# Kernel tuning notes

Measured on AMD Instinct MI355X. Metric: run time of the kernel, lower is better.

Reference implementation:

```python
import jax, jax.numpy as jnp
from jax import lax
import numpy as np

TOP_K = 2
CAPACITY_FACTOR = 1.0


def setup_inputs() -> dict:
    key = jax.random.key(0)
    kx, kg, k1, k2 = jax.random.split(key, 4)
    B, S, D, F, E = 8, 4096, 512, 1024, 16
    x = jax.random.normal(kx, (B, S, D), dtype=jnp.float32)
    w_gate = jax.random.normal(kg, (D, E), dtype=jnp.float32) * 0.02
    w1 = jax.random.normal(k1, (E, D, 2 * F), dtype=jnp.float32) * 0.02
    w2 = jax.random.normal(k2, (E, F, D), dtype=jnp.float32) * 0.02
    return {"x": x, "w_gate": w_gate, "w1": w1, "w2": w2}


def reference(x, w_gate, w1, w2):
    # Inference mode: no gating noise, dropout is identity.
    B, S, D = x.shape
    E = w_gate.shape[1]
    T = B * S
    capacity = max(1, int(CAPACITY_FACTOR * T / E))  # static

    flat = x.reshape(T, D)
    gate_logits = flat @ w_gate                      # [T, E]
    gate_scores = jax.nn.softmax(gate_logits, axis=-1)
    topk_vals, topk_idx = lax.top_k(gate_scores, TOP_K)  # [T, k]

    phi_mean = gate_scores.mean(axis=0)
    aux_loss = E * jnp.sum(phi_mean * phi_mean)

    # Per-expert combine weight for every token: [E, T]
    onehot = topk_idx[None, :, :] == jnp.arange(E)[:, None, None]  # [E, T, k]
    w_et = jnp.sum(jnp.where(onehot, topk_vals[None], 0.0), axis=-1)  # [E, T]

    # Capacity truncation: keep the `capacity` highest-weight tokens per expert
    sel_w, sel_idx = lax.top_k(w_et, capacity)  # [E, C]; unrouted picks have weight 0

    xs = flat[sel_idx]                                  # [E, C, D] gather
    h = jnp.einsum('ecd,edf->ecf', xs, w1)              # [E, C, 2F]
    h1, h2 = jnp.split(h, 2, axis=-1)
    act = h1 * jax.nn.silu(h2)                          # SwiGLU
    out_e = jnp.einsum('ecf,efd->ecd', act, w2) * sel_w[..., None]  # [E, C, D]

    combined = jnp.zeros((T, D), dtype=flat.dtype).at[sel_idx.reshape(-1)].add(
        out_e.reshape(-1, D))
    return combined.reshape(B, S, D), aux_loss
```

## Files before the change

### kernel.cpp

```cpp
#include <hip/hip_runtime.h>
#include <hip/hip_bf16.h>
#include <math.h>

#define T_TOK 32768
#define D_DIM 512
#define E_EXP 16
#define F_DIM 1024
#define C_CAP 2048

typedef __attribute__((ext_vector_type(8))) __bf16 bf16x8;
typedef __attribute__((ext_vector_type(4))) float f32x4;

__device__ __forceinline__ unsigned short f2bf(float f) {
  unsigned u = __float_as_uint(f);
  u += 0x7FFFu + ((u >> 16) & 1u);
  return (unsigned short)(u >> 16);
}

__device__ __forceinline__ void gld16(const void* gptr, void* ldsptr) {
  __builtin_amdgcn_global_load_lds(
      (__attribute__((address_space(1))) void*)(void*)gptr,
      (__attribute__((address_space(3))) void*)ldsptr, 16, 0, 0);
}

__global__ void transpose_conv_kernel(const float* __restrict__ in,
                                      unsigned short* __restrict__ out,
                                      int R, int Cc) {
  __shared__ float tile[32][33];
  int e = blockIdx.z;
  int r0 = blockIdx.y * 32, c0 = blockIdx.x * 32;
  const float* pin = in + (size_t)e * R * Cc;
  unsigned short* pout = out + (size_t)e * R * Cc;
  int tx = threadIdx.x, ty = threadIdx.y;
  #pragma unroll
  for (int i = 0; i < 32; i += 8)
    tile[ty + i][tx] = pin[(size_t)(r0 + ty + i) * Cc + c0 + tx];
  __syncthreads();
  #pragma unroll
  for (int i = 0; i < 32; i += 8)
    pout[(size_t)(c0 + ty + i) * R + r0 + tx] = f2bf(tile[tx][ty + i]);
}

__global__ __launch_bounds__(256) void gate_kernel(
    const float* __restrict__ x, const float* __restrict__ wg,
    float* __restrict__ w_et, float* __restrict__ phi_sum,
    unsigned short* __restrict__ xb) {
  __shared__ float wgl[D_DIM * E_EXP];
  __shared__ float phil[E_EXP];
  int tid = threadIdx.x;
  for (int i = tid; i < D_DIM * E_EXP; i += 256) wgl[i] = wg[i];
  if (tid < E_EXP) phil[tid] = 0.f;
  __syncthreads();

  int g = tid >> 4;
  int e = tid & 15;
  int t = blockIdx.x * 16 + g;

  float acc = 0.f;
  const float* xr = x + (size_t)t * D_DIM;
  #pragma unroll 4
  for (int d = 0; d < D_DIM; d += 4) {
    float4 xv = *(const float4*)(xr + d);
    acc = fmaf(xv.x, wgl[(d + 0) * 16 + e], acc);
    acc = fmaf(xv.y, wgl[(d + 1) * 16 + e], acc);
    acc = fmaf(xv.z, wgl[(d + 2) * 16 + e], acc);
    acc = fmaf(xv.w, wgl[(d + 3) * 16 + e], acc);
  }

  unsigned short* xrow = xb + (size_t)t * D_DIM;
  #pragma unroll
  for (int j = 0; j < 8; ++j) {
    int idx = j * 16 + e;
    float4 v = *(const float4*)(xr + idx * 4);
    ushort4 o;
    o.x = f2bf(v.x); o.y = f2bf(v.y); o.z = f2bf(v.z); o.w = f2bf(v.w);
    ((ushort4*)xrow)[idx] = o;
  }

  float m = acc;
  for (int off = 8; off; off >>= 1) m = fmaxf(m, __shfl_xor(m, off));
  float p = expf(acc - m);
  float s = p;
  for (int off = 8; off; off >>= 1) s += __shfl_xor(s, off);
  float score = p / s;
  atomicAdd(&phil[e], score);

  float v1 = score; int i1 = e;
  for (int off = 8; off; off >>= 1) {
    float ov = __shfl_xor(v1, off); int oi = __shfl_xor(i1, off);
    if (ov > v1 || (ov == v1 && oi < i1)) { v1 = ov; i1 = oi; }
  }
  float sc2 = (e == i1) ? -1.f : score;
  float v2 = sc2; int i2 = e;
  for (int off = 8; off; off >>= 1) {
    float ov = __shfl_xor(v2, off); int oi = __shfl_xor(i2, off);
    if (ov > v2 || (ov == v2 && oi < i2)) { v2 = ov; i2 = oi; }
  }
  if (e == 0) {
    w_et[(size_t)i1 * T_TOK + t] = v1;
    w_et[(size_t)i2 * T_TOK + t] = v2;
  }
  __syncthreads();
  if (tid < E_EXP) atomicAdd(&phi_sum[tid], phil[tid]);
}

__global__ void aux_kernel(const float* __restrict__ phi_sum, float* __restrict__ out_aux) {
  if (threadIdx.x == 0) {
    float s = 0.f;
    for (int e = 0; e < E_EXP; ++e) {
      float pm = phi_sum[e] / (float)T_TOK;
      s += pm * pm;
    }
    *out_aux = (float)E_EXP * s;
  }
}

__global__ __launch_bounds__(1024) void select_kernel(
    const float* __restrict__ w_et, int* __restrict__ sel_idx, float* __restrict__ sel_w) {
  int e = blockIdx.x, tid = threadIdx.x;
  const float* w = w_et + (size_t)e * T_TOK;
  __shared__ unsigned hist[256];
  __shared__ unsigned scan_buf[1024];
  __shared__ unsigned sh_prefix, sh_k, sh_ngt, sh_cnt;

  unsigned prefix = 0, k = C_CAP, n_gt = 0;
  for (int pass = 0; pass < 4; ++pass) {
    int shift = 24 - pass * 8;
    if (tid < 256) hist[tid] = 0;
    if (tid == 0) sh_cnt = 0;
    __syncthreads();
    for (int i = tid; i < T_TOK; i += 1024) {
      unsigned b = __float_as_uint(w[i]);
      bool match = (pass == 0) || ((b >> (shift + 8)) == (prefix >> (shift + 8)));
      if (match) atomicAdd(&hist[(b >> shift) & 0xFFu], 1u);
    }
    __syncthreads();
    if (tid == 0) {
      unsigned cum = 0; int b = 255;
      for (; b > 0; --b) {
        unsigned c = hist[b];
        if (cum + c >= k) break;
        cum += c;
      }
      sh_prefix = prefix | ((unsigned)b << shift);
      sh_k = k - cum;
      sh_ngt = n_gt + cum;
    }
    __syncthreads();
    prefix = sh_prefix; k = sh_k; n_gt = sh_ngt;
    __syncthreads();
  }

  unsigned thr = prefix;
  unsigned eq_take = k;
  int base = tid * 32;

  unsigned myeq = 0;
  for (int i = base; i < base + 32; ++i) {
    float v = w[i];
    unsigned b = __float_as_uint(v);
    if (b > thr) {
      unsigned pos = atomicAdd(&sh_cnt, 1u);
      sel_idx[(size_t)e * C_CAP + pos] = i;
      sel_w[(size_t)e * C_CAP + pos] = v;
    } else if (b == thr) {
      myeq++;
    }
  }
  scan_buf[tid] = myeq;
  __syncthreads();
  for (int off = 1; off < 1024; off <<= 1) {
    unsigned add = (tid >= off) ? scan_buf[tid - off] : 0u;
    __syncthreads();
    scan_buf[tid] += add;
    __syncthreads();
  }
  unsigned excl = scan_buf[tid] - myeq;

  if (thr != 0u) {
    unsigned r = excl;
    for (int i = base; i < base + 32 && r < eq_take; ++i) {
      unsigned b = __float_as_uint(w[i]);
      if (b == thr) {
        sel_idx[(size_t)e * C_CAP + n_gt + r] = i;
        sel_w[(size_t)e * C_CAP + n_gt + r] = w[i];
        r++;
      }
    }
  }
  unsigned m_e = (thr != 0u) ? (unsigned)C_CAP : n_gt;
  for (unsigned i = m_e + tid; i < C_CAP; i += 1024) {
    sel_idx[(size_t)e * C_CAP + i] = 0;
    sel_w[(size_t)e * C_CAP + i] = 0.f;
  }
}

__global__ __launch_bounds__(256) void gemm1_kernel(
    const unsigned short* __restrict__ xb,
    const unsigned short* __restrict__ w1t,
    const int* __restrict__ sel_idx,
    unsigned short* __restrict__ act) {
  __shared__ __align__(16) unsigned short As[128 * 64];
  __shared__ __align__(16) unsigned short Bs[128 * 64];
  int bid = (blockIdx.x & 7) * 512 + (blockIdx.x >> 3);
  int nt = bid & 15, mt = (bid >> 4) & 15, e = bid >> 8;
  int tid = threadIdx.x, lane = tid & 63, wid = tid >> 6;

  const unsigned short* ag[4];
  const unsigned short* bg[4];
  unsigned lofs[4];
  #pragma unroll
  for (int s = 0; s < 4; ++s) {
    int c = s * 256 + tid;
    int row = c >> 3, kc = c & 7;
    int kcs = kc ^ (row & 7);
    int tok = sel_idx[e * C_CAP + mt * 128 + row];
    ag[s] = xb + (size_t)tok * D_DIM + kcs * 8;
    int hcol = (row < 64) ? (nt * 64 + row) : (F_DIM + nt * 64 + (row - 64));
    bg[s] = w1t + ((size_t)e * 2 * F_DIM + hcol) * D_DIM + kcs * 8;
    lofs[s] = (unsigned)(s * 256 + wid * 64) * 16;
  }

  f32x4 zero = {0.f, 0.f, 0.f, 0.f};
  f32x4 acc[2][8];
  #pragma unroll
  for (int m = 0; m < 2; ++m)
    #pragma unroll
    for (int n = 0; n < 8; ++n) acc[m][n] = zero;

  int cl = lane & 15, rg = lane >> 4;
  int sw = cl & 7;

  for (int kt = 0; kt < D_DIM / 64; ++kt) {
    #pragma unroll
    for (int s = 0; s < 4; ++s) {
      gld16(ag[s] + kt * 64, (char*)As + lofs[s]);
      gld16(bg[s] + kt * 64, (char*)Bs + lofs[s]);
    }
    __syncthreads();
    #pragma unroll
    for (int kk = 0; kk < 64; kk += 32) {
      int cofs = (((kk >> 3) + rg) ^ sw) << 3;
      bf16x8 a[2], b[8];
      #pragma unroll
      for (int m = 0; m < 2; ++m)
        a[m] = *(const bf16x8*)&As[(wid * 32 + m * 16 + cl) * 64 + cofs];
      #pragma unroll
      for (int n = 0; n < 8; ++n)
        b[n] = *(const bf16x8*)&Bs[(n * 16 + cl) * 64 + cofs];
      #pragma unroll
      for (int m = 0; m < 2; ++m)
        #pragma unroll
        for (int n = 0; n < 8; ++n)
          acc[m][n] = __builtin_amdgcn_mfma_f32_16x16x32_bf16(a[m], b[n], acc[m][n], 0, 0, 0);
    }
    __syncthreads();
  }

  #pragma unroll
  for (int m = 0; m < 2; ++m) {
    #pragma unroll
    for (int n = 0; n < 4; ++n) {
      #pragma unroll
      for (int r = 0; r < 4; ++r) {
        int row = mt * 128 + wid * 32 + m * 16 + rg * 4 + r;
        int col = nt * 64 + n * 16 + cl;
        float h1 = acc[m][n][r];
        float h2 = acc[m][n + 4][r];
        float sg = h2 / (1.f + __expf(-h2));
        act[((size_t)e * C_CAP + row) * F_DIM + col] = f2bf(h1 * sg);
      }
    }
  }
}

__global__ __launch_bounds__(256) void gemm2_kernel(
    const unsigned short* __restrict__ act,
    const unsigned short* __restrict__ w2t,
    const int* __restrict__ sel_idx,
    const float* __restrict__ sel_w,
    float* __restrict__ out) {
  __shared__ __align__(16) unsigned short As[128 * 64];
  __shared__ __align__(16) unsigned short Bs[128 * 64];
  int bid = (blockIdx.x & 7) * 128 + (blockIdx.x >> 3);
  int nt = bid & 3, mt = (bid >> 2) & 15, e = bid >> 6;
  int tid = threadIdx.x, lane = tid & 63, wid = tid >> 6;
  int wr = wid >> 1, wc = wid & 1;

  const unsigned short* ag[4];
  const unsigned short* bg[4];
  unsigned lofs[4];
  #pragma unroll
  for (int s = 0; s < 4; ++s) {
    int c = s * 256 + tid;
    int row = c >> 3, kc = c & 7;
    int kcs = kc ^ (row & 7);
    ag[s] = act + ((size_t)e * C_CAP + mt * 128 + row) * F_DIM + kcs * 8;
    int dcol = nt * 128 + row;
    bg[s] = w2t + ((size_t)e * D_DIM + dcol) * F_DIM + kcs * 8;
    lofs[s] = (unsigned)(s * 256 + wid * 64) * 16;
  }

  f32x4 zero = {0.f, 0.f, 0.f, 0.f};
  f32x4 acc[4][4];
  #pragma unroll
  for (int m = 0; m < 4; ++m)
    #pragma unroll
    for (int n = 0; n < 4; ++n) acc[m][n] = zero;

  int cl = lane & 15, rg = lane >> 4;
  int sw = cl & 7;

  for (int kt = 0; kt < F_DIM / 64; ++kt) {
    #pragma unroll
    for (int s = 0; s < 4; ++s) {
      gld16(ag[s] + kt * 64, (char*)As + lofs[s]);
      gld16(bg[s] + kt * 64, (char*)Bs + lofs[s]);
    }
    __syncthreads();
    #pragma unroll
    for (int kk = 0; kk < 64; kk += 32) {
      int cofs = (((kk >> 3) + rg) ^ sw) << 3;
      bf16x8 a[4], b[4];
      #pragma unroll
      for (int m = 0; m < 4; ++m)
        a[m] = *(const bf16x8*)&As[(wr * 64 + m * 16 + cl) * 64 + cofs];
      #pragma unroll
      for (int n = 0; n < 4; ++n)
        b[n] = *(const bf16x8*)&Bs[(wc * 64 + n * 16 + cl) * 64 + cofs];
      #pragma unroll
      for (int m = 0; m < 4; ++m)
        #pragma unroll
        for (int n = 0; n < 4; ++n)
          acc[m][n] = __builtin_amdgcn_mfma_f32_16x16x32_bf16(a[m], b[n], acc[m][n], 0, 0, 0);
    }
    __syncthreads();
  }

  #pragma unroll
  for (int m = 0; m < 4; ++m) {
    #pragma unroll
    for (int r = 0; r < 4; ++r) {
      int slot = mt * 128 + wr * 64 + m * 16 + rg * 4 + r;
      float wgt = sel_w[e * C_CAP + slot];
      int tok = sel_idx[e * C_CAP + slot];
      float* orow = out + (size_t)tok * D_DIM;
      #pragma unroll
      for (int n = 0; n < 4; ++n) {
        int col = nt * 128 + wc * 64 + n * 16 + cl;
        atomicAdd(&orow[col], acc[m][n][r] * wgt);
      }
    }
  }
}

extern "C" void kernel_launch(void* const* d_in, const int* in_sizes, int n_in,
                              void* d_out, int out_size, void* d_ws, size_t ws_size,
                              hipStream_t stream) {
  const float* x  = (const float*)d_in[0];
  const float* wg = (const float*)d_in[1];
  const float* w1 = (const float*)d_in[2];
  const float* w2 = (const float*)d_in[3];
  float* out = (float*)d_out;

  char* ws = (char*)d_ws;
  size_t off = 0;
  auto carve = [&](size_t bytes) -> void* {
    void* p = ws + off;
    off += (bytes + 255) & ~(size_t)255;
    return p;
  };
  float* w_et            = (float*)carve((size_t)E_EXP * T_TOK * 4);
  float* phi             = (float*)carve(64);
  int* sel_i             = (int*)carve((size_t)E_EXP * C_CAP * 4);
  float* sel_wv          = (float*)carve((size_t)E_EXP * C_CAP * 4);
  unsigned short* xb     = (unsigned short*)carve((size_t)T_TOK * D_DIM * 2);
  unsigned short* w1t    = (unsigned short*)carve((size_t)E_EXP * 2 * F_DIM * D_DIM * 2);
  unsigned short* w2t    = (unsigned short*)carve((size_t)E_EXP * D_DIM * F_DIM * 2);
  unsigned short* actb   = (unsigned short*)carve((size_t)E_EXP * C_CAP * F_DIM * 2);
  if (off > ws_size) return;

  hipMemsetAsync(w_et, 0, (size_t)E_EXP * T_TOK * 4, stream);
  hipMemsetAsync(phi, 0, 64, stream);
  hipMemsetAsync(d_out, 0, (size_t)out_size * 4, stream);

  transpose_conv_kernel<<<dim3(2 * F_DIM / 32, D_DIM / 32, E_EXP), dim3(32, 8), 0, stream>>>(
      w1, w1t, D_DIM, 2 * F_DIM);
  transpose_conv_kernel<<<dim3(D_DIM / 32, F_DIM / 32, E_EXP), dim3(32, 8), 0, stream>>>(
      w2, w2t, F_DIM, D_DIM);
  gate_kernel<<<T_TOK / 16, 256, 0, stream>>>(x, wg, w_et, phi, xb);
  select_kernel<<<E_EXP, 1024, 0, stream>>>(w_et, sel_i, sel_wv);
  aux_kernel<<<1, 64, 0, stream>>>(phi, out + (size_t)T_TOK * D_DIM);
  gemm1_kernel<<<E_EXP * 16 * 16, 256, 0, stream>>>(xb, w1t, sel_i, actb);
  gemm2_kernel<<<E_EXP * 16 * 4, 256, 0, stream>>>(actb, w2t, sel_i, sel_wv, out);
}
```

Measured before the change: 410.6 us.

## Double-buffer LDS tiles in expert GEMMs and streamline top-capacity selection

Both expert GEMM kernels now keep two LDS buffers per operand. The global-to-LDS loads for the next K tile are issued before the MFMA work on the current tile, so memory latency can overlap with compute. The selection kernel now uses per-wave histograms to cut LDS atomic contention, and replaces the 1024-step barrier scan and the atomic slot counter with a wave-shuffle prefix scan over packed greater-than and equal counts, which writes deterministic slot positions. The cost is double the LDS per GEMM block, which may lower occupancy.

```diff
diff --git a/kernel.cpp b/kernel.cpp
--- a/kernel.cpp
+++ b/kernel.cpp
@@ -118,27 +118,35 @@
 __global__ __launch_bounds__(1024) void select_kernel(
     const float* __restrict__ w_et, int* __restrict__ sel_idx, float* __restrict__ sel_w) {
   int e = blockIdx.x, tid = threadIdx.x;
+  int lane = tid & 63, wv = tid >> 6;
   const float* w = w_et + (size_t)e * T_TOK;
-  __shared__ unsigned hist[256];
-  __shared__ unsigned scan_buf[1024];
-  __shared__ unsigned sh_prefix, sh_k, sh_ngt, sh_cnt;
+  __shared__ unsigned hist[16][256];
+  __shared__ unsigned red[256];
+  __shared__ unsigned wsum[16];
+  __shared__ unsigned sh_prefix, sh_k, sh_ngt;
 
   unsigned prefix = 0, k = C_CAP, n_gt = 0;
   for (int pass = 0; pass < 4; ++pass) {
     int shift = 24 - pass * 8;
-    if (tid < 256) hist[tid] = 0;
-    if (tid == 0) sh_cnt = 0;
+    for (int i = tid; i < 16 * 256; i += 1024) ((unsigned*)hist)[i] = 0;
     __syncthreads();
     for (int i = tid; i < T_TOK; i += 1024) {
       unsigned b = __float_as_uint(w[i]);
       bool match = (pass == 0) || ((b >> (shift + 8)) == (prefix >> (shift + 8)));
-      if (match) atomicAdd(&hist[(b >> shift) & 0xFFu], 1u);
+      if (match) atomicAdd(&hist[wv][(b >> shift) & 0xFFu], 1u);
+    }
+    __syncthreads();
+    if (tid < 256) {
+      unsigned t = 0;
+      #pragma unroll
+      for (int wq = 0; wq < 16; ++wq) t += hist[wq][tid];
+      red[tid] = t;
     }
     __syncthreads();
     if (tid == 0) {
       unsigned cum = 0; int b = 255;
       for (; b > 0; --b) {
-        unsigned c = hist[b];
+        unsigned c = red[b];
         if (cum + c >= k) break;
         cum += c;
       }
@@ -155,43 +163,41 @@
   unsigned eq_take = k;
   int base = tid * 32;
 
-  unsigned myeq = 0;
+  unsigned mygt = 0, myeq = 0;
+  for (int i = base; i < base + 32; ++i) {
+    unsigned b = __float_as_uint(w[i]);
+    if (b > thr) mygt++;
+    else if (b == thr) myeq++;
+  }
+  unsigned val = (mygt << 16) | myeq;
+  unsigned inc = val;
+  #pragma unroll
+  for (int off = 1; off < 64; off <<= 1) {
+    unsigned o = __shfl_up(inc, off);
+    if (lane >= off) inc += o;
+  }
+  if (lane == 63) wsum[wv] = inc;
+  __syncthreads();
+  if (tid == 0) {
+    unsigned c = 0;
+    #pragma unroll
+    for (int q = 0; q < 16; ++q) { unsigned t = wsum[q]; wsum[q] = c; c += t; }
+  }
+  __syncthreads();
+  unsigned excl = wsum[wv] + inc - val;
+  unsigned rgt = excl >> 16;
+  unsigned req = excl & 0xFFFFu;
+
+  int* si = sel_idx + (size_t)e * C_CAP;
+  float* swp = sel_w + (size_t)e * C_CAP;
   for (int i = base; i < base + 32; ++i) {
     float v = w[i];
     unsigned b = __float_as_uint(v);
     if (b > thr) {
-      unsigned pos = atomicAdd(&sh_cnt, 1u);
-      sel_idx[(size_t)e * C_CAP + pos] = i;
-      sel_w[(size_t)e * C_CAP + pos] = v;
-    } else if (b == thr) {
-      myeq++;
-    }
-  }
-  scan_buf[tid] = myeq;
-  __syncthreads();
-  for (int off = 1; off < 1024; off <<= 1) {
-    unsigned add = (tid >= off) ? scan_buf[tid - off] : 0u;
-    __syncthreads();
-    scan_buf[tid] += add;
-    __syncthreads();
-  }
-  unsigned excl = scan_buf[tid] - myeq;
-
-  if (thr != 0u) {
-    unsigned r = excl;
-    for (int i = base; i < base + 32 && r < eq_take; ++i) {
-      unsigned b = __float_as_uint(w[i]);
-      if (b == thr) {
-        sel_idx[(size_t)e * C_CAP + n_gt + r] = i;
-        sel_w[(size_t)e * C_CAP + n_gt + r] = w[i];
-        r++;
-      }
-    }
-  }
-  unsigned m_e = (thr != 0u) ? (unsigned)C_CAP : n_gt;
-  for (unsigned i = m_e + tid; i < C_CAP; i += 1024) {
-    sel_idx[(size_t)e * C_CAP + i] = 0;
-    sel_w[(size_t)e * C_CAP + i] = 0.f;
+      si[rgt] = i; swp[rgt] = v; rgt++;
+    } else if (b == thr && req < eq_take) {
+      si[n_gt + req] = i; swp[n_gt + req] = v; req++;
+    }
   }
 }
 
@@ -200,8 +206,8 @@
     const unsigned short* __restrict__ w1t,
     const int* __restrict__ sel_idx,
     unsigned short* __restrict__ act) {
-  __shared__ __align__(16) unsigned short As[128 * 64];
-  __shared__ __align__(16) unsigned short Bs[128 * 64];
+  __shared__ __align__(16) unsigned short As[2][128 * 64];
+  __shared__ __align__(16) unsigned short Bs[2][128 * 64];
   int bid = (blockIdx.x & 7) * 512 + (blockIdx.x >> 3);
   int nt = bid & 15, mt = (bid >> 4) & 15, e = bid >> 8;
   int tid = threadIdx.x, lane = tid & 63, wid = tid >> 6;
@@ -231,23 +237,33 @@
   int cl = lane & 15, rg = lane >> 4;
   int sw = cl & 7;
 
-  for (int kt = 0; kt < D_DIM / 64; ++kt) {
-    #pragma unroll
-    for (int s = 0; s < 4; ++s) {
-      gld16(ag[s] + kt * 64, (char*)As + lofs[s]);
-      gld16(bg[s] + kt * 64, (char*)Bs + lofs[s]);
-    }
-    __syncthreads();
+  #pragma unroll
+  for (int s = 0; s < 4; ++s) {
+    gld16(ag[s], (char*)As[0] + lofs[s]);
+    gld16(bg[s], (char*)Bs[0] + lofs[s]);
+  }
+  __syncthreads();
+
+  const int NK = D_DIM / 64;
+  for (int kt = 0; kt < NK; ++kt) {
+    int cur = kt & 1;
+    if (kt + 1 < NK) {
+      #pragma unroll
+      for (int s = 0; s < 4; ++s) {
+        gld16(ag[s] + (kt + 1) * 64, (char*)As[cur ^ 1] + lofs[s]);
+        gld16(bg[s] + (kt + 1) * 64, (char*)Bs[cur ^ 1] + lofs[s]);
+      }
+    }
     #pragma unroll
     for (int kk = 0; kk < 64; kk += 32) {
       int cofs = (((kk >> 3) + rg) ^ sw) << 3;
       bf16x8 a[2], b[8];
       #pragma unroll
       for (int m = 0; m < 2; ++m)
-        a[m] = *(const bf16x8*)&As[(wid * 32 + m * 16 + cl) * 64 + cofs];
+        a[m] = *(const bf16x8*)&As[cur][(wid * 32 + m * 16 + cl) * 64 + cofs];
       #pragma unroll
       for (int n = 0; n < 8; ++n)
-        b[n] = *(const bf16x8*)&Bs[(n * 16 + cl) * 64 + cofs];
+        b[n] = *(const bf16x8*)&Bs[cur][(n * 16 + cl) * 64 + cofs];
       #pragma unroll
       for (int m = 0; m < 2; ++m)
         #pragma unroll
@@ -280,8 +296,8 @@
     const int* __restrict__ sel_idx,
     const float* __restrict__ sel_w,
     float* __restrict__ out) {
-  __shared__ __align__(16) unsigned short As[128 * 64];
-  __shared__ __align__(16) unsigned short Bs[128 * 64];
+  __shared__ __align__(16) unsigned short As[2][128 * 64];
+  __shared__ __align__(16) unsigned short Bs[2][128 * 64];
   int bid = (blockIdx.x & 7) * 128 + (blockIdx.x >> 3);
   int nt = bid & 3, mt = (bid >> 2) & 15, e = bid >> 6;
   int tid = threadIdx.x, lane = tid & 63, wid = tid >> 6;
@@ -311,23 +327,33 @@
   int cl = lane & 15, rg = lane >> 4;
   int sw = cl & 7;
 
-  for (int kt = 0; kt < F_DIM / 64; ++kt) {
-    #pragma unroll
-    for (int s = 0; s < 4; ++s) {
-      gld16(ag[s] + kt * 64, (char*)As + lofs[s]);
-      gld16(bg[s] + kt * 64, (char*)Bs + lofs[s]);
-    }
-    __syncthreads();
+  #pragma unroll
+  for (int s = 0; s < 4; ++s) {
+    gld16(ag[s], (char*)As[0] + lofs[s]);
+    gld16(bg[s], (char*)Bs[0] + lofs[s]);
+  }
+  __syncthreads();
+
+  const int NK = F_DIM / 64;
+  for (int kt = 0; kt < NK; ++kt) {
+    int cur = kt & 1;
+    if (kt + 1 < NK) {
+      #pragma unroll
+      for (int s = 0; s < 4; ++s) {
+        gld16(ag[s] + (kt + 1) * 64, (char*)As[cur ^ 1] + lofs[s]);
+        gld16(bg[s] + (kt + 1) * 64, (char*)Bs[cur ^ 1] + lofs[s]);
+      }
+    }
     #pragma unroll
     for (int kk = 0; kk < 64; kk += 32) {
       int cofs = (((kk >> 3) + rg) ^ sw) << 3;
       bf16x8 a[4], b[4];
       #pragma unroll
       for (int m = 0; m < 4; ++m)
-        a[m] = *(const bf16x8*)&As[(wr * 64 + m * 16 + cl) * 64 + cofs];
+        a[m] = *(const bf16x8*)&As[cur][(wr * 64 + m * 16 + cl) * 64 + cofs];
       #pragma unroll
       for (int n = 0; n < 4; ++n)
-        b[n] = *(const bf16x8*)&Bs[(wc * 64 + n * 16 + cl) * 64 + cofs];
+        b[n] = *(const bf16x8*)&Bs[cur][(wc * 64 + n * 16 + cl) * 64 + cofs];
       #pragma unroll
       for (int m = 0; m < 4; ++m)
         #pragma unroll
```

Result: faster. 400.0 us (-2.6%).
